# Performance work log

Hardware: AMD Instinct MI355X
Metric: run time of the kernel (lower is better)

Reference implementation:

```python
import jax, jax.numpy as jnp
import numpy as np

FP8_MAX = 448.0


def setup_inputs() -> dict:
    key = jax.random.key(0)
    kx, kw = jax.random.split(key)
    in_features, out_features = 1024, 1024
    x = jax.random.normal(kx, (32768, in_features), dtype=jnp.float32)
    # kaiming_uniform_ with a=sqrt(5): bound = sqrt(6/((1+a^2)*fan_in)) = sqrt(1/fan_in)
    bound = 1.0 / np.sqrt(in_features)
    weight = jax.random.uniform(kw, (out_features, in_features), dtype=jnp.float32,
                                minval=-bound, maxval=bound)
    bias = jnp.zeros((out_features,), dtype=jnp.float32)
    return {"x": x, "weight": weight, "bias": bias}


def reference(x, weight, bias):
    # per-tensor input quant
    input_scale = jnp.maximum(jnp.max(jnp.abs(x)) / FP8_MAX, 1e-12)
    x_q = jnp.round(jnp.clip(x / input_scale, -FP8_MAX, FP8_MAX))
    # per-output-channel weight quant
    weight_amax = jnp.max(jnp.abs(weight), axis=1)            # [out]
    weight_scale = jnp.maximum(weight_amax / FP8_MAX, 1e-12)  # [out]
    weight_q = jnp.round(jnp.clip(weight / weight_scale[:, None], -FP8_MAX, FP8_MAX))
    # integer-valued GEMM in fp32, then dequant + bias
    output_q = jnp.einsum('ti,oi->to', x_q, weight_q)          # [T, out]
    output = output_q * (input_scale * weight_scale)[None, :]
    return output + bias
```

## Files before the change

kernel.cpp:

```cpp
#include <hip/hip_runtime.h>
#include <hip/hip_fp16.h>

#define FP8_MAX 448.0f
#define M_ 32768
#define N_ 1024
#define K_ 1024
#define BM 128
#define BN 128
#define BK 64

typedef _Float16 f16x8 __attribute__((ext_vector_type(8)));
typedef _Float16 f16x4 __attribute__((ext_vector_type(4)));
typedef float f32x4 __attribute__((ext_vector_type(4)));

__device__ inline void gload_lds16(const void* g, void* l) {
    __builtin_amdgcn_global_load_lds(
        (const __attribute__((address_space(1))) void*)g,
        (__attribute__((address_space(3))) void*)l,
        16, 0, 0);
}

__global__ __launch_bounds__(256) void prep_kernel(const float* __restrict__ x,
                                                   const float* __restrict__ w,
                                                   unsigned* __restrict__ amax_bits,
                                                   float* __restrict__ wscale,
                                                   _Float16* __restrict__ wq,
                                                   int n) {
    __shared__ float sm[4];
    if (blockIdx.x < 1024) {
        int row = blockIdx.x;
        const float4* wr4 = (const float4*)(w + (size_t)row * K_);
        float4 v = wr4[threadIdx.x];
        float m = fmaxf(fmaxf(fabsf(v.x), fabsf(v.y)), fmaxf(fabsf(v.z), fabsf(v.w)));
        #pragma unroll
        for (int off = 32; off > 0; off >>= 1)
            m = fmaxf(m, __shfl_down(m, off, 64));
        if ((threadIdx.x & 63) == 0) sm[threadIdx.x >> 6] = m;
        __syncthreads();
        m = fmaxf(fmaxf(sm[0], sm[1]), fmaxf(sm[2], sm[3]));
        float scale = fmaxf(m / FP8_MAX, 1e-12f);
        if (threadIdx.x == 0) wscale[row] = scale;
        float inv = 1.0f / scale;
        f16x4 o;
        o[0] = (_Float16)rintf(fminf(fmaxf(v.x * inv, -FP8_MAX), FP8_MAX));
        o[1] = (_Float16)rintf(fminf(fmaxf(v.y * inv, -FP8_MAX), FP8_MAX));
        o[2] = (_Float16)rintf(fminf(fmaxf(v.z * inv, -FP8_MAX), FP8_MAX));
        o[3] = (_Float16)rintf(fminf(fmaxf(v.w * inv, -FP8_MAX), FP8_MAX));
        ((f16x4*)(wq + (size_t)row * K_))[threadIdx.x] = o;
    } else {
        float m = 0.0f;
        const float4* x4 = (const float4*)x;
        int n4 = n >> 2;
        int stride = 2048 * 256;
        for (int i = (blockIdx.x - 1024) * 256 + threadIdx.x; i < n4; i += stride) {
            float4 v = x4[i];
            m = fmaxf(m, fmaxf(fmaxf(fabsf(v.x), fabsf(v.y)),
                               fmaxf(fabsf(v.z), fabsf(v.w))));
        }
        #pragma unroll
        for (int off = 32; off > 0; off >>= 1)
            m = fmaxf(m, __shfl_down(m, off, 64));
        if ((threadIdx.x & 63) == 0) sm[threadIdx.x >> 6] = m;
        __syncthreads();
        if (threadIdx.x == 0) {
            float b = fmaxf(fmaxf(sm[0], sm[1]), fmaxf(sm[2], sm[3]));
            atomicMax(amax_bits, __float_as_uint(b));
        }
    }
}

__global__ __launch_bounds__(256) void quant_x_kernel(const float* __restrict__ x,
                                                      const unsigned* __restrict__ amax_bits,
                                                      _Float16* __restrict__ xq,
                                                      int n) {
    float amax = __uint_as_float(*amax_bits);
    float scale = fmaxf(amax / FP8_MAX, 1e-12f);
    float inv = 1.0f / scale;
    const float4* x4 = (const float4*)x;
    f16x4* o4 = (f16x4*)xq;
    int n4 = n >> 2;
    int stride = gridDim.x * blockDim.x;
    for (int i = blockIdx.x * blockDim.x + threadIdx.x; i < n4; i += stride) {
        float4 v = x4[i];
        f16x4 o;
        o[0] = (_Float16)rintf(fminf(fmaxf(v.x * inv, -FP8_MAX), FP8_MAX));
        o[1] = (_Float16)rintf(fminf(fmaxf(v.y * inv, -FP8_MAX), FP8_MAX));
        o[2] = (_Float16)rintf(fminf(fmaxf(v.z * inv, -FP8_MAX), FP8_MAX));
        o[3] = (_Float16)rintf(fminf(fmaxf(v.w * inv, -FP8_MAX), FP8_MAX));
        o4[i] = o;
    }
}

__global__ __launch_bounds__(256) void gemm_kernel(const _Float16* __restrict__ xq,
                                                   const _Float16* __restrict__ wq,
                                                   const unsigned* __restrict__ amax_bits,
                                                   const float* __restrict__ wscale,
                                                   const float* __restrict__ bias,
                                                   float* __restrict__ out) {
    __shared__ __align__(16) _Float16 sA[BM * BK];
    __shared__ __align__(16) _Float16 sB[BN * BK];

    const int tid  = threadIdx.x;
    const int wave = tid >> 6;
    const int lane = tid & 63;
    const int q = lane >> 4;
    const int r = lane & 15;
    const int r7 = r & 7;
    const int wm = (wave >> 1) * 64;
    const int wn = (wave & 1) * 64;

    const int m0 = (int)(blockIdx.x & 255) * BM;
    const int n0 = (int)(blockIdx.x >> 8) * BN;

    const int trow = tid >> 3;
    const int tcol = (((tid & 7) ^ (trow & 7)) * 8);

    const _Float16* Ag = xq + ((size_t)(m0 + trow)) * K_ + tcol;
    const _Float16* Bg = wq + ((size_t)(n0 + trow)) * K_ + tcol;
    char* lA = (char*)sA + wave * 1024;
    char* lB = (char*)sB + wave * 1024;

    f32x4 acc[4][4] = {};

    for (int kt = 0; kt < K_; kt += BK) {
        #pragma unroll
        for (int rr = 0; rr < 4; ++rr) {
            gload_lds16(Ag + kt + (size_t)(rr * 32) * K_, lA + rr * 4096);
            gload_lds16(Bg + kt + (size_t)(rr * 32) * K_, lB + rr * 4096);
        }
        __syncthreads();
        #pragma unroll
        for (int kk = 0; kk < BK; kk += 32) {
            f16x8 a[4], b[4];
            const int chunk = q + (kk >> 3);
            const int pos = (chunk ^ r7) * 8;
            #pragma unroll
            for (int i = 0; i < 4; ++i)
                a[i] = *(const f16x8*)&sA[(wm + i * 16 + r) * BK + pos];
            #pragma unroll
            for (int j = 0; j < 4; ++j)
                b[j] = *(const f16x8*)&sB[(wn + j * 16 + r) * BK + pos];
            #pragma unroll
            for (int i = 0; i < 4; ++i)
                #pragma unroll
                for (int j = 0; j < 4; ++j)
                    acc[i][j] = __builtin_amdgcn_mfma_f32_16x16x32_f16(a[i], b[j], acc[i][j], 0, 0, 0);
        }
        __syncthreads();
    }

    float amax = __uint_as_float(*amax_bits);
    float iscale = fmaxf(amax / FP8_MAX, 1e-12f);

    #pragma unroll
    for (int j = 0; j < 4; ++j) {
        int col = n0 + wn + j * 16 + r;
        float sc = iscale * wscale[col];
        float bs = bias[col];
        #pragma unroll
        for (int i = 0; i < 4; ++i) {
            int rowb = m0 + wm + i * 16 + q * 4;
            #pragma unroll
            for (int t = 0; t < 4; ++t)
                out[(size_t)(rowb + t) * N_ + col] = acc[i][j][t] * sc + bs;
        }
    }
}

extern "C" void kernel_launch(void* const* d_in, const int* in_sizes, int n_in,
                              void* d_out, int out_size, void* d_ws, size_t ws_size,
                              hipStream_t stream) {
    const float* x    = (const float*)d_in[0];
    const float* w    = (const float*)d_in[1];
    const float* bias = (const float*)d_in[2];
    float* out = (float*)d_out;

    char* ws = (char*)d_ws;
    unsigned* amax_bits = (unsigned*)ws;
    float* wscale       = (float*)(ws + 256);
    _Float16* xq        = (_Float16*)(ws + 8192);
    _Float16* wq        = (_Float16*)(ws + 8192 + (size_t)M_ * K_ * 2);

    hipMemsetAsync(amax_bits, 0, 4, stream);
    prep_kernel<<<3072, 256, 0, stream>>>(x, w, amax_bits, wscale, wq, M_ * K_);
    quant_x_kernel<<<8192, 256, 0, stream>>>(x, amax_bits, xq, M_ * K_);
    gemm_kernel<<<2048, 256, 0, stream>>>(xq, wq, amax_bits, wscale, bias, out);
}
```

Baseline: 374.0 us.

## Switch GEMM to 32x32x16 MFMA and replace atomic amax with partial reduction

The GEMM inner loop now uses 32x32x16 f16 MFMA tiles (2x2 per wave) instead of 16x16x32 tiles (4x4 per wave), with the LDS fragment indexing and epilogue row mapping reworked to match. Each output tile now needs fewer MFMA issues and fragment loads. The global max of x is no longer taken with a float atomicMax plus a memset; per-block partial maxima are written out and each quant block re-reduces the 2048 partials, then stores the scale once. This removes the memset launch and atomic contention but adds a small redundant reduction in every quant block.

```diff
diff --git a/kernel.cpp b/kernel.cpp
--- a/kernel.cpp
+++ b/kernel.cpp
@@ -11,7 +11,7 @@
 
 typedef _Float16 f16x8 __attribute__((ext_vector_type(8)));
 typedef _Float16 f16x4 __attribute__((ext_vector_type(4)));
-typedef float f32x4 __attribute__((ext_vector_type(4)));
+typedef float f32x16 __attribute__((ext_vector_type(16)));
 
 __device__ inline void gload_lds16(const void* g, void* l) {
     __builtin_amdgcn_global_load_lds(
@@ -22,7 +22,7 @@
 
 __global__ __launch_bounds__(256) void prep_kernel(const float* __restrict__ x,
                                                    const float* __restrict__ w,
-                                                   unsigned* __restrict__ amax_bits,
+                                                   float* __restrict__ xamax_part,
                                                    float* __restrict__ wscale,
                                                    _Float16* __restrict__ wq,
                                                    int n) {
@@ -63,19 +63,33 @@
         if ((threadIdx.x & 63) == 0) sm[threadIdx.x >> 6] = m;
         __syncthreads();
         if (threadIdx.x == 0) {
-            float b = fmaxf(fmaxf(sm[0], sm[1]), fmaxf(sm[2], sm[3]));
-            atomicMax(amax_bits, __float_as_uint(b));
+            xamax_part[blockIdx.x - 1024] =
+                fmaxf(fmaxf(sm[0], sm[1]), fmaxf(sm[2], sm[3]));
         }
     }
 }
 
 __global__ __launch_bounds__(256) void quant_x_kernel(const float* __restrict__ x,
-                                                      const unsigned* __restrict__ amax_bits,
+                                                      const float* __restrict__ xamax_part,
+                                                      float* __restrict__ xscale_out,
                                                       _Float16* __restrict__ xq,
                                                       int n) {
-    float amax = __uint_as_float(*amax_bits);
+    __shared__ float sm[4];
+    const float4* p4 = (const float4*)xamax_part;
+    float4 a = p4[threadIdx.x];
+    float4 b = p4[threadIdx.x + 256];
+    float m = fmaxf(fmaxf(fmaxf(a.x, a.y), fmaxf(a.z, a.w)),
+                    fmaxf(fmaxf(b.x, b.y), fmaxf(b.z, b.w)));
+    #pragma unroll
+    for (int off = 32; off > 0; off >>= 1)
+        m = fmaxf(m, __shfl_down(m, off, 64));
+    if ((threadIdx.x & 63) == 0) sm[threadIdx.x >> 6] = m;
+    __syncthreads();
+    float amax = fmaxf(fmaxf(sm[0], sm[1]), fmaxf(sm[2], sm[3]));
     float scale = fmaxf(amax / FP8_MAX, 1e-12f);
+    if (threadIdx.x == 0) xscale_out[0] = scale;
     float inv = 1.0f / scale;
+
     const float4* x4 = (const float4*)x;
     f16x4* o4 = (f16x4*)xq;
     int n4 = n >> 2;
@@ -93,7 +107,7 @@
 
 __global__ __launch_bounds__(256) void gemm_kernel(const _Float16* __restrict__ xq,
                                                    const _Float16* __restrict__ wq,
-                                                   const unsigned* __restrict__ amax_bits,
+                                                   const float* __restrict__ xscale,
                                                    const float* __restrict__ wscale,
                                                    const float* __restrict__ bias,
                                                    float* __restrict__ out) {
@@ -103,9 +117,9 @@
     const int tid  = threadIdx.x;
     const int wave = tid >> 6;
     const int lane = tid & 63;
-    const int q = lane >> 4;
-    const int r = lane & 15;
-    const int r7 = r & 7;
+    const int h   = lane >> 5;
+    const int m32 = lane & 31;
+    const int m7  = m32 & 7;
     const int wm = (wave >> 1) * 64;
     const int wn = (wave & 1) * 64;
 
@@ -120,7 +134,7 @@
     char* lA = (char*)sA + wave * 1024;
     char* lB = (char*)sB + wave * 1024;
 
-    f32x4 acc[4][4] = {};
+    f32x16 acc[2][2] = {};
 
     for (int kt = 0; kt < K_; kt += BK) {
         #pragma unroll
@@ -130,39 +144,40 @@
         }
         __syncthreads();
         #pragma unroll
-        for (int kk = 0; kk < BK; kk += 32) {
-            f16x8 a[4], b[4];
-            const int chunk = q + (kk >> 3);
-            const int pos = (chunk ^ r7) * 8;
-            #pragma unroll
-            for (int i = 0; i < 4; ++i)
-                a[i] = *(const f16x8*)&sA[(wm + i * 16 + r) * BK + pos];
-            #pragma unroll
-            for (int j = 0; j < 4; ++j)
-                b[j] = *(const f16x8*)&sB[(wn + j * 16 + r) * BK + pos];
-            #pragma unroll
-            for (int i = 0; i < 4; ++i)
+        for (int ks = 0; ks < 4; ++ks) {
+            f16x8 a[2], b[2];
+            const int chunk = ks * 2 + h;
+            const int pos = (chunk ^ m7) * 8;
+            #pragma unroll
+            for (int i = 0; i < 2; ++i)
+                a[i] = *(const f16x8*)&sA[(wm + i * 32 + m32) * BK + pos];
+            #pragma unroll
+            for (int j = 0; j < 2; ++j)
+                b[j] = *(const f16x8*)&sB[(wn + j * 32 + m32) * BK + pos];
+            #pragma unroll
+            for (int i = 0; i < 2; ++i)
                 #pragma unroll
-                for (int j = 0; j < 4; ++j)
-                    acc[i][j] = __builtin_amdgcn_mfma_f32_16x16x32_f16(a[i], b[j], acc[i][j], 0, 0, 0);
-        }
-        __syncthreads();
-    }
-
-    float amax = __uint_as_float(*amax_bits);
-    float iscale = fmaxf(amax / FP8_MAX, 1e-12f);
+                for (int j = 0; j < 2; ++j)
+                    acc[i][j] = __builtin_amdgcn_mfma_f32_32x32x16_f16(a[i], b[j], acc[i][j], 0, 0, 0);
+        }
+        __syncthreads();
+    }
+
+    float iscale = xscale[0];
 
     #pragma unroll
-    for (int j = 0; j < 4; ++j) {
-        int col = n0 + wn + j * 16 + r;
+    for (int j = 0; j < 2; ++j) {
+        int col = n0 + wn + j * 32 + m32;
         float sc = iscale * wscale[col];
         float bs = bias[col];
         #pragma unroll
-        for (int i = 0; i < 4; ++i) {
-            int rowb = m0 + wm + i * 16 + q * 4;
-            #pragma unroll
-            for (int t = 0; t < 4; ++t)
-                out[(size_t)(rowb + t) * N_ + col] = acc[i][j][t] * sc + bs;
+        for (int i = 0; i < 2; ++i) {
+            int rb = m0 + wm + i * 32 + 4 * h;
+            #pragma unroll
+            for (int reg = 0; reg < 16; ++reg) {
+                int row = rb + (reg & 3) + 8 * (reg >> 2);
+                out[(size_t)row * N_ + col] = acc[i][j][reg] * sc + bs;
+            }
         }
     }
 }
@@ -176,13 +191,13 @@
     float* out = (float*)d_out;
 
     char* ws = (char*)d_ws;
-    unsigned* amax_bits = (unsigned*)ws;
-    float* wscale       = (float*)(ws + 256);
-    _Float16* xq        = (_Float16*)(ws + 8192);
-    _Float16* wq        = (_Float16*)(ws + 8192 + (size_t)M_ * K_ * 2);
-
-    hipMemsetAsync(amax_bits, 0, 4, stream);
-    prep_kernel<<<3072, 256, 0, stream>>>(x, w, amax_bits, wscale, wq, M_ * K_);
-    quant_x_kernel<<<8192, 256, 0, stream>>>(x, amax_bits, xq, M_ * K_);
-    gemm_kernel<<<2048, 256, 0, stream>>>(xq, wq, amax_bits, wscale, bias, out);
-}
+    float* xscale      = (float*)ws;
+    float* xamax_part  = (float*)(ws + 1024);
+    float* wscale      = (float*)(ws + 16384);
+    _Float16* wq       = (_Float16*)(ws + 32768);
+    _Float16* xq       = (_Float16*)(ws + (4u << 20));
+
+    prep_kernel<<<3072, 256, 0, stream>>>(x, w, xamax_part, wscale, wq, M_ * K_);
+    quant_x_kernel<<<8192, 256, 0, stream>>>(x, xamax_part, xscale, xq, M_ * K_);
+    gemm_kernel<<<2048, 256, 0, stream>>>(xq, wq, xscale, wscale, bias, out);
+}
```

New measurement: 341.4 us. 1.1x faster.
